# Optimization experiments

Measured on AMD Instinct MI355X. Metric: run time of the kernel, lower is better.

The kernel has to match this reference:

```python
import jax, jax.numpy as jnp
import numpy as np

EMB_DIM = 128
NUM_NODES = 200000
NUM_EDGES = 1000000


def setup_inputs() -> dict:
    key = jax.random.key(0)
    k1, k2, k3 = jax.random.split(key, 3)
    node_emb = jax.random.normal(k1, (NUM_NODES, 2 * EMB_DIM), dtype=jnp.float32)
    rel_emb = jax.random.normal(k2, (1, 2 * EMB_DIM), dtype=jnp.float32)
    edge_label_index = jax.random.randint(k3, (2, NUM_EDGES), 0, NUM_NODES, dtype=jnp.int64)
    return {"node_emb": node_emb, "rel_emb": rel_emb, "edge_label_index": edge_label_index}


def reference(node_emb, rel_emb, edge_label_index):
    D = EMB_DIM
    # gather head/tail rows: [E, 2D]
    head = node_emb[edge_label_index[0]]
    tail = node_emb[edge_label_index[1]]
    head_re, head_im = head[:, :D], head[:, D:]
    tail_re, tail_im = tail[:, :D], tail[:, D:]
    rel = rel_emb[0]  # single edge type
    rel_re, rel_im = rel[:D], rel[D:]
    # ComplEx score: Re(<h, r, conj(t)>)
    h = ((head_re * rel_re * tail_re)
         + (head_im * rel_re * tail_im)
         + (head_re * rel_im * tail_im)
         - (head_im * rel_im * tail_re)).sum(axis=-1)  # [E]
    return h
```

## Files before the change

### kernel.cpp

```cpp
#include <hip/hip_runtime.h>

#define EMB_D 128

__global__ __launch_bounds__(256) void pack_int8_kernel(
    const float* __restrict__ node_emb,
    uint2*       __restrict__ tab,
    float*       __restrict__ scales,
    int num_nodes)
{
    const int j   = threadIdx.x & 31;
    const int hw  = (blockIdx.x * blockDim.x + threadIdx.x) >> 5;
    const int nHW = (gridDim.x * blockDim.x) >> 5;

    for (int n = hw; n < num_nodes; n += nHW) {
        const float* rowp = node_emb + (size_t)n * (2 * EMB_D);
        const float4 re = *reinterpret_cast<const float4*>(rowp + 4 * j);
        const float4 im = *reinterpret_cast<const float4*>(rowp + EMB_D + 4 * j);

        float m = fmaxf(fmaxf(fmaxf(fabsf(re.x), fabsf(re.y)), fmaxf(fabsf(re.z), fabsf(re.w))),
                        fmaxf(fmaxf(fabsf(im.x), fabsf(im.y)), fmaxf(fabsf(im.z), fabsf(im.w))));
        #pragma unroll
        for (int off = 1; off <= 16; off <<= 1)
            m = fmaxf(m, __shfl_xor(m, off, 64));

        const float inv = (m > 0.f) ? 127.0f / m : 0.f;

        #define Q(x) ((unsigned)((int)rintf((x) * inv)) & 255u)
        const unsigned lo = Q(re.x) | (Q(im.x) << 8) | (Q(re.y) << 16) | (Q(im.y) << 24);
        const unsigned hi = Q(re.z) | (Q(im.z) << 8) | (Q(re.w) << 16) | (Q(im.w) << 24);
        #undef Q

        tab[(size_t)n * 32 + j] = make_uint2(lo, hi);
        if (j == 0) scales[n] = m * (1.0f / 127.0f);
    }
}

__device__ __forceinline__ float score4_i8(const uint2 hq, const uint2 tq,
                                           const float4 rr, const float4 ri) {
    union U { uint2 u; signed char c[8]; };
    U H, T; H.u = hq; T.u = tq;
    float acc = 0.f;
#define DIM_TERM(d, C) { \
        const float hr = (float)H.c[2*(d)], hi = (float)H.c[2*(d)+1]; \
        const float tr = (float)T.c[2*(d)], ti = (float)T.c[2*(d)+1]; \
        acc += rr.C * (hr * tr + hi * ti) + ri.C * (hr * ti - hi * tr); }
    DIM_TERM(0, x) DIM_TERM(1, y) DIM_TERM(2, z) DIM_TERM(3, w)
#undef DIM_TERM
    return acc;
}

__global__ __launch_bounds__(256) void complex_score_i8_kernel(
    const uint2* __restrict__ tab,
    const float* __restrict__ scales,
    const float* __restrict__ rel_emb,
    const int*   __restrict__ idx,
    float*       __restrict__ out,
    int num_edges)
{
    const int lane = threadIdx.x & 63;
    const int j    = lane & 31;
    const int sub  = lane >> 5;

    const float4 rr = reinterpret_cast<const float4*>(rel_emb)[j];
    const float4 ri = reinterpret_cast<const float4*>(rel_emb + EMB_D)[j];

    const int w      = blockIdx.x * (blockDim.x >> 6) + (threadIdx.x >> 6);
    const int nWaves = gridDim.x * (blockDim.x >> 6);
    const int nTiles = num_edges >> 3;

    for (int tile = w; tile < nTiles; tile += nWaves) {
        const int base = tile << 3;
        const int4 h03 = *reinterpret_cast<const int4*>(idx + base);
        const int4 h47 = *reinterpret_cast<const int4*>(idx + base + 4);
        const int4 t03 = *reinterpret_cast<const int4*>(idx + num_edges + base);
        const int4 t47 = *reinterpret_cast<const int4*>(idx + num_edges + base + 4);

        const int h0 = sub ? h03.y : h03.x;
        const int h1 = sub ? h03.w : h03.z;
        const int h2_ = sub ? h47.y : h47.x;
        const int h3_ = sub ? h47.w : h47.z;
        const int t0 = sub ? t03.y : t03.x;
        const int t1 = sub ? t03.w : t03.z;
        const int t2_ = sub ? t47.y : t47.x;
        const int t3_ = sub ? t47.w : t47.z;

        const uint2 hv0 = tab[(size_t)h0  * 32 + j];
        const uint2 tv0 = tab[(size_t)t0  * 32 + j];
        const uint2 hv1 = tab[(size_t)h1  * 32 + j];
        const uint2 tv1 = tab[(size_t)t1  * 32 + j];
        const uint2 hv2 = tab[(size_t)h2_ * 32 + j];
        const uint2 tv2 = tab[(size_t)t2_ * 32 + j];
        const uint2 hv3 = tab[(size_t)h3_ * 32 + j];
        const uint2 tv3 = tab[(size_t)t3_ * 32 + j];
        const float s0 = scales[h0] * scales[t0];
        const float s1 = scales[h1] * scales[t1];
        const float s2 = scales[h2_] * scales[t2_];
        const float s3 = scales[h3_] * scales[t3_];

        float acc0 = score4_i8(hv0, tv0, rr, ri);
        float acc1 = score4_i8(hv1, tv1, rr, ri);
        float acc2 = score4_i8(hv2, tv2, rr, ri);
        float acc3 = score4_i8(hv3, tv3, rr, ri);

        #pragma unroll
        for (int off = 1; off <= 16; off <<= 1) {
            acc0 += __shfl_xor(acc0, off, 64);
            acc1 += __shfl_xor(acc1, off, 64);
            acc2 += __shfl_xor(acc2, off, 64);
            acc3 += __shfl_xor(acc3, off, 64);
        }

        if (j == 0) {
            out[base + 0 + sub] = acc0 * s0;
            out[base + 2 + sub] = acc1 * s1;
            out[base + 4 + sub] = acc2 * s2;
            out[base + 6 + sub] = acc3 * s3;
        }
    }

    const int tailStart = nTiles << 3;
    if (w == 0 && tailStart < num_edges) {
        for (int e = tailStart + sub; e < num_edges; e += 2) {
            const int h = idx[e], t = idx[num_edges + e];
            float acc = score4_i8(tab[(size_t)h * 32 + j], tab[(size_t)t * 32 + j], rr, ri);
            #pragma unroll
            for (int off = 1; off <= 16; off <<= 1) acc += __shfl_xor(acc, off, 64);
            if (j == 0) out[e] = acc * scales[h] * scales[t];
        }
    }
}

__global__ __launch_bounds__(256) void complex_score_f32_kernel(
    const float* __restrict__ node_emb, const float* __restrict__ rel_emb,
    const int* __restrict__ idx, float* __restrict__ out, int num_edges)
{
    const int lane = threadIdx.x & 63;
    const int j = lane & 31, sub = lane >> 5;
    const float4 rr = reinterpret_cast<const float4*>(rel_emb)[j];
    const float4 ri = reinterpret_cast<const float4*>(rel_emb + EMB_D)[j];
    const int w = blockIdx.x * (blockDim.x >> 6) + (threadIdx.x >> 6);
    const int nWaves = gridDim.x * (blockDim.x >> 6);
    for (int e = 2 * w + sub; e < num_edges; e += 2 * nWaves) {
        const int h = idx[e], t = idx[num_edges + e];
        const float4* hp = reinterpret_cast<const float4*>(node_emb + (size_t)h * (2 * EMB_D));
        const float4* tp = reinterpret_cast<const float4*>(node_emb + (size_t)t * (2 * EMB_D));
        const float4 hr = hp[j], hi = hp[32 + j], tr = tp[j], ti = tp[32 + j];
        float acc;
        acc  = rr.x * (hr.x * tr.x + hi.x * ti.x) + ri.x * (hr.x * ti.x - hi.x * tr.x);
        acc += rr.y * (hr.y * tr.y + hi.y * ti.y) + ri.y * (hr.y * ti.y - hi.y * tr.y);
        acc += rr.z * (hr.z * tr.z + hi.z * ti.z) + ri.z * (hr.z * ti.z - hi.z * tr.z);
        acc += rr.w * (hr.w * tr.w + hi.w * ti.w) + ri.w * (hr.w * ti.w - hi.w * tr.w);
        #pragma unroll
        for (int off = 1; off <= 16; off <<= 1) acc += __shfl_xor(acc, off, 64);
        if (j == 0) out[e] = acc;
    }
}

extern "C" void kernel_launch(void* const* d_in, const int* in_sizes, int n_in,
                              void* d_out, int out_size, void* d_ws, size_t ws_size,
                              hipStream_t stream) {
    const float* node_emb = (const float*)d_in[0];
    const float* rel_emb  = (const float*)d_in[1];
    const int*   idx      = (const int*)d_in[2];
    float*       out      = (float*)d_out;

    const int num_nodes = in_sizes[0] / (2 * EMB_D);
    const int num_edges = in_sizes[2] / 2;

    const size_t tab_bytes = (size_t)num_nodes * 256;
    const size_t need      = tab_bytes + (size_t)num_nodes * sizeof(float);
    const bool idx_ok      = (num_edges % 4) == 0;

    if (ws_size >= need && idx_ok) {
        uint2* tab    = (uint2*)d_ws;
        float* scales = (float*)((char*)d_ws + tab_bytes);
        pack_int8_kernel<<<2048, 256, 0, stream>>>(node_emb, tab, scales, num_nodes);
        complex_score_i8_kernel<<<2048, 256, 0, stream>>>(tab, scales, rel_emb, idx, out, num_edges);
    } else {
        complex_score_f32_kernel<<<2048, 256, 0, stream>>>(node_emb, rel_emb, idx, out, num_edges);
    }
}
```

Measured before the change: 132.2 us.

## Bucket-sort edges by head node before gathering int8 embeddings

Adds histogram, scan and scatter kernels that bucket edges by head-node range (128 nodes per bucket) into records carrying head, tail, edge id and a precomputed scale product. The gather kernel then processes edges in bucketed order with contiguous per-block tile ranges, so head-row reads of the int8 table get more cache locality. In exchange it adds four extra launches, global atomics, a 16-byte-per-edge record buffer write and read, and scattered output writes.

```diff
diff --git a/kernel.cpp b/kernel.cpp
--- a/kernel.cpp
+++ b/kernel.cpp
@@ -1,6 +1,8 @@
 #include <hip/hip_runtime.h>
 
-#define EMB_D 128
+#define EMB_D  128
+#define NBMAX  2048
+#define BSHIFT 7
 
 __global__ __launch_bounds__(256) void pack_int8_kernel(
     const float* __restrict__ node_emb,
@@ -32,6 +34,72 @@
 
         tab[(size_t)n * 32 + j] = make_uint2(lo, hi);
         if (j == 0) scales[n] = m * (1.0f / 127.0f);
+    }
+}
+
+__global__ __launch_bounds__(256) void init_kernel(
+    int* __restrict__ hist, int nb,
+    int4* __restrict__ rec, int E, int paddedE)
+{
+    const int i = blockIdx.x * blockDim.x + threadIdx.x;
+    if (i < nb) hist[i] = 0;
+    if (i < paddedE - E) rec[E + i] = make_int4(0, 0, 0x7fffffff, 0);
+}
+
+__global__ __launch_bounds__(256) void hist_kernel(
+    const int* __restrict__ heads, int E, int* __restrict__ hist, int nb)
+{
+    __shared__ int lh[NBMAX];
+    for (int i = threadIdx.x; i < nb; i += 256) lh[i] = 0;
+    __syncthreads();
+    for (int e = blockIdx.x * blockDim.x + threadIdx.x; e < E; e += gridDim.x * blockDim.x)
+        atomicAdd(&lh[heads[e] >> BSHIFT], 1);
+    __syncthreads();
+    for (int i = threadIdx.x; i < nb; i += 256) {
+        const int v = lh[i];
+        if (v) atomicAdd(&hist[i], v);
+    }
+}
+
+__global__ __launch_bounds__(256) void scan_kernel(
+    const int* __restrict__ hist, int* __restrict__ cursor, int nb)
+{
+    __shared__ int sums[256];
+    int local[8];
+    const int base = threadIdx.x * 8;
+    int s = 0;
+    #pragma unroll
+    for (int k = 0; k < 8; ++k) {
+        const int i = base + k;
+        const int v = (i < nb) ? hist[i] : 0;
+        local[k] = s; s += v;
+    }
+    sums[threadIdx.x] = s;
+    __syncthreads();
+    if (threadIdx.x == 0) {
+        int a = 0;
+        for (int i = 0; i < 256; ++i) { const int t = sums[i]; sums[i] = a; a += t; }
+    }
+    __syncthreads();
+    const int off = sums[threadIdx.x];
+    #pragma unroll
+    for (int k = 0; k < 8; ++k) {
+        const int i = base + k;
+        if (i < nb) cursor[i] = off + local[k];
+    }
+}
+
+__global__ __launch_bounds__(256) void scatter_kernel(
+    const int* __restrict__ idx, int E,
+    const float* __restrict__ scales,
+    int* __restrict__ cursor, int4* __restrict__ rec)
+{
+    for (int e = blockIdx.x * blockDim.x + threadIdx.x; e < E; e += gridDim.x * blockDim.x) {
+        const int h = idx[e];
+        const int t = idx[E + e];
+        const float s = scales[h] * scales[t];
+        const int pos = atomicAdd(&cursor[h >> BSHIFT], 1);
+        rec[pos] = make_int4(h, t, e, __float_as_int(s));
     }
 }
 
@@ -49,13 +117,12 @@
     return acc;
 }
 
-__global__ __launch_bounds__(256) void complex_score_i8_kernel(
+__global__ __launch_bounds__(256) void gather_sorted_kernel(
     const uint2* __restrict__ tab,
-    const float* __restrict__ scales,
+    const int4*  __restrict__ rec,
     const float* __restrict__ rel_emb,
-    const int*   __restrict__ idx,
     float*       __restrict__ out,
-    int num_edges)
+    int num_edges, int nTiles)
 {
     const int lane = threadIdx.x & 63;
     const int j    = lane & 31;
@@ -64,38 +131,26 @@
     const float4 rr = reinterpret_cast<const float4*>(rel_emb)[j];
     const float4 ri = reinterpret_cast<const float4*>(rel_emb + EMB_D)[j];
 
-    const int w      = blockIdx.x * (blockDim.x >> 6) + (threadIdx.x >> 6);
-    const int nWaves = gridDim.x * (blockDim.x >> 6);
-    const int nTiles = num_edges >> 3;
-
-    for (int tile = w; tile < nTiles; tile += nWaves) {
+    const int tilesPerBlock = (nTiles + (int)gridDim.x - 1) / (int)gridDim.x;
+    const int tBeg = blockIdx.x * tilesPerBlock;
+    const int tEnd = min(tBeg + tilesPerBlock, nTiles);
+    const int wid  = threadIdx.x >> 6;
+
+    for (int tile = tBeg + wid; tile < tEnd; tile += 4) {
         const int base = tile << 3;
-        const int4 h03 = *reinterpret_cast<const int4*>(idx + base);
-        const int4 h47 = *reinterpret_cast<const int4*>(idx + base + 4);
-        const int4 t03 = *reinterpret_cast<const int4*>(idx + num_edges + base);
-        const int4 t47 = *reinterpret_cast<const int4*>(idx + num_edges + base + 4);
-
-        const int h0 = sub ? h03.y : h03.x;
-        const int h1 = sub ? h03.w : h03.z;
-        const int h2_ = sub ? h47.y : h47.x;
-        const int h3_ = sub ? h47.w : h47.z;
-        const int t0 = sub ? t03.y : t03.x;
-        const int t1 = sub ? t03.w : t03.z;
-        const int t2_ = sub ? t47.y : t47.x;
-        const int t3_ = sub ? t47.w : t47.z;
-
-        const uint2 hv0 = tab[(size_t)h0  * 32 + j];
-        const uint2 tv0 = tab[(size_t)t0  * 32 + j];
-        const uint2 hv1 = tab[(size_t)h1  * 32 + j];
-        const uint2 tv1 = tab[(size_t)t1  * 32 + j];
-        const uint2 hv2 = tab[(size_t)h2_ * 32 + j];
-        const uint2 tv2 = tab[(size_t)t2_ * 32 + j];
-        const uint2 hv3 = tab[(size_t)h3_ * 32 + j];
-        const uint2 tv3 = tab[(size_t)t3_ * 32 + j];
-        const float s0 = scales[h0] * scales[t0];
-        const float s1 = scales[h1] * scales[t1];
-        const float s2 = scales[h2_] * scales[t2_];
-        const float s3 = scales[h3_] * scales[t3_];
+        const int4 r0 = rec[base + 0 + sub];
+        const int4 r1 = rec[base + 2 + sub];
+        const int4 r2 = rec[base + 4 + sub];
+        const int4 r3 = rec[base + 6 + sub];
+
+        const uint2 hv0 = tab[(size_t)r0.x * 32 + j];
+        const uint2 tv0 = tab[(size_t)r0.y * 32 + j];
+        const uint2 hv1 = tab[(size_t)r1.x * 32 + j];
+        const uint2 tv1 = tab[(size_t)r1.y * 32 + j];
+        const uint2 hv2 = tab[(size_t)r2.x * 32 + j];
+        const uint2 tv2 = tab[(size_t)r2.y * 32 + j];
+        const uint2 hv3 = tab[(size_t)r3.x * 32 + j];
+        const uint2 tv3 = tab[(size_t)r3.y * 32 + j];
 
         float acc0 = score4_i8(hv0, tv0, rr, ri);
         float acc1 = score4_i8(hv1, tv1, rr, ri);
@@ -111,21 +166,10 @@
         }
 
         if (j == 0) {
-            out[base + 0 + sub] = acc0 * s0;
-            out[base + 2 + sub] = acc1 * s1;
-            out[base + 4 + sub] = acc2 * s2;
-            out[base + 6 + sub] = acc3 * s3;
-        }
-    }
-
-    const int tailStart = nTiles << 3;
-    if (w == 0 && tailStart < num_edges) {
-        for (int e = tailStart + sub; e < num_edges; e += 2) {
-            const int h = idx[e], t = idx[num_edges + e];
-            float acc = score4_i8(tab[(size_t)h * 32 + j], tab[(size_t)t * 32 + j], rr, ri);
-            #pragma unroll
-            for (int off = 1; off <= 16; off <<= 1) acc += __shfl_xor(acc, off, 64);
-            if (j == 0) out[e] = acc * scales[h] * scales[t];
+            if (r0.z < num_edges) out[r0.z] = acc0 * __int_as_float(r0.w);
+            if (r1.z < num_edges) out[r1.z] = acc1 * __int_as_float(r1.w);
+            if (r2.z < num_edges) out[r2.z] = acc2 * __int_as_float(r2.w);
+            if (r3.z < num_edges) out[r3.z] = acc3 * __int_as_float(r3.w);
         }
     }
 }
@@ -167,15 +211,31 @@
     const int num_nodes = in_sizes[0] / (2 * EMB_D);
     const int num_edges = in_sizes[2] / 2;
 
-    const size_t tab_bytes = (size_t)num_nodes * 256;
-    const size_t need      = tab_bytes + (size_t)num_nodes * sizeof(float);
-    const bool idx_ok      = (num_edges % 4) == 0;
-
-    if (ws_size >= need && idx_ok) {
+    const int nb      = ((num_nodes - 1) >> BSHIFT) + 1;
+    const int paddedE = (num_edges + 7) & ~7;
+    const int nTiles  = paddedE >> 3;
+
+    const size_t tab_b   = (size_t)num_nodes * 256;
+    const size_t sc_b    = (size_t)num_nodes * sizeof(float);
+    const size_t rec_off = (tab_b + sc_b + 15) & ~(size_t)15;
+    const size_t rec_b   = (size_t)paddedE * sizeof(int4);
+    const size_t hist_off = rec_off + rec_b;
+    const size_t need     = hist_off + 2 * (size_t)NBMAX * sizeof(int);
+
+    if (ws_size >= need && nb <= NBMAX && num_edges >= 8) {
         uint2* tab    = (uint2*)d_ws;
-        float* scales = (float*)((char*)d_ws + tab_bytes);
+        float* scales = (float*)((char*)d_ws + tab_b);
+        int4*  rec    = (int4*)((char*)d_ws + rec_off);
+        int*   hist   = (int*)((char*)d_ws + hist_off);
+        int*   cursor = hist + NBMAX;
+
+        init_kernel<<<8, 256, 0, stream>>>(hist, nb, rec, num_edges, paddedE);
         pack_int8_kernel<<<2048, 256, 0, stream>>>(node_emb, tab, scales, num_nodes);
-        complex_score_i8_kernel<<<2048, 256, 0, stream>>>(tab, scales, rel_emb, idx, out, num_edges);
+        hist_kernel<<<256, 256, 0, stream>>>(idx, num_edges, hist, nb);
+        scan_kernel<<<1, 256, 0, stream>>>(hist, cursor, nb);
+        scatter_kernel<<<512, 256, 0, stream>>>(idx, num_edges, scales, cursor, rec);
+        gather_sorted_kernel<<<2048, 256, 0, stream>>>(tab, rec, rel_emb, out,
+                                                       num_edges, nTiles);
     } else {
         complex_score_f32_kernel<<<2048, 256, 0, stream>>>(node_emb, rel_emb, idx, out, num_edges);
     }
```

Measured after the change: 294.2 us. 122% more time.
